# Optimization experiments

Measured on AMD Instinct MI355X. Metric: run time of the kernel, lower is better.

## Reference

```python
import jax, jax.numpy as jnp
import numpy as np

B, H, W, C, F = 32, 32, 32, 256, 64
K_NEIGH = 32  # L1 pixel-distance cutoff used for the static mask


def _distance_mask(h, w, k):
    # coords: [hw, 2] of (y, x); L1 pixel distances, normalized by max(h, w)
    ys, xs = jnp.meshgrid(jnp.arange(h), jnp.arange(w), indexing='ij')
    coords = jnp.stack([ys, xs], axis=-1).reshape(-1, 2).astype(jnp.float32)
    diff = jnp.abs(coords[:, None, :] - coords[None, :, :]).sum(-1)  # [hw, hw], == cdist p=1
    dist = diff / float(max(h, w))
    return jnp.where(diff <= k, dist, 0.0)


def setup_inputs() -> dict:
    key = jax.random.key(0)
    ks = jax.random.split(key, 7)
    return {
        'feature_map': jax.random.normal(ks[0], (B, H, W, C), dtype=jnp.float32),
        'emb_W': jax.random.normal(ks[1], (F, C), dtype=jnp.float32) * (1.0 / np.sqrt(C)),
        'emb_b': jax.random.normal(ks[2], (F,), dtype=jnp.float32) * 0.01,
        'attn_W': jax.random.normal(ks[3], (C, C), dtype=jnp.float32) * (1.0 / np.sqrt(C)),
        'attn_b': jax.random.normal(ks[4], (C,), dtype=jnp.float32) * 0.01,
        'thr_W': jax.random.normal(ks[5], (1, C), dtype=jnp.float32) * (1.0 / np.sqrt(C)),
        'thr_b': jax.random.normal(ks[6], (1,), dtype=jnp.float32) * 0.01,
        'layer': 0,
    }


def reference(feature_map, emb_W, emb_b, attn_W, attn_b, thr_W, thr_b, layer):
    b, h, w, c = feature_map.shape
    hw = h * w
    x = feature_map.reshape(b, hw, c)  # row-major (y, x) flatten, matches torch view

    # 1x1 conv -> per-pixel linear: instance embeddings [b, hw, F]
    emb = jnp.einsum('bnc,fc->bnf', x, emb_W) + emb_b

    # squared Euclidean pairwise distances (cdist p=2, then squared)
    sq = jnp.sum(emb * emb, axis=-1)  # [b, hw]
    d2 = jnp.maximum(sq[:, :, None] + sq[:, None, :]
                     - 2.0 * jnp.einsum('bnf,bmf->bnm', emb, emb), 0.0)

    mask = _distance_mask(h, w, K_NEIGH)  # [hw, hw] static buffer
    sim = jax.nn.softmax(jnp.exp(-d2) - (1.0 - mask), axis=-1)  # [b, hw, hw]

    # shortcut = attention_conv(feature_map): [b, hw, c]
    shortcut = jnp.einsum('bnc,dc->bnd', x, attn_W) + attn_b

    # per-pixel learned threshold: [b, hw]
    Tinst = (jnp.einsum('bnc,oc->bno', shortcut, thr_W) + thr_b)[..., 0]

    A = jax.nn.softmax(jnp.maximum(sim - Tinst[:, None, :], 0.0), axis=-1)

    # bmm: out[b, i, c] = sum_j shortcut[b, j, c] * A[b, i, j]
    attn_out = jnp.einsum('bjc,bij->bic', shortcut, A)

    res = (x + attn_out).reshape(b, h, w, c)
    return res
```

## Files before the change

kernel.cpp:

```cpp
#include <hip/hip_runtime.h>
#include <hip/hip_bf16.h>


typedef short bf16x8 __attribute__((ext_vector_type(8)));
typedef float f32x4 __attribute__((ext_vector_type(4)));

#define LOG2E 1.4426950408889634f

__device__ __forceinline__ unsigned short f2bf(float f) {
  unsigned u = __float_as_uint(f);
  u += 0x7fffu + ((u >> 16) & 1u);
  return (unsigned short)(u >> 16);
}
__device__ __forceinline__ float bf2f(unsigned short h) {
  return __uint_as_float(((unsigned)h) << 16);
}
__device__ __forceinline__ unsigned pack2(float a, float b) {
  return (unsigned)f2bf(a) | ((unsigned)f2bf(b) << 16);
}
__device__ __forceinline__ unsigned cvtpk(float lo, float hi) {
  unsigned r;
  asm("v_cvt_pk_bf16_f32 %0, %1, %2" : "=v"(r) : "v"(lo), "v"(hi));
  return r;
}
__device__ __forceinline__ float exp2x(float x) {
  float r;
  asm("v_exp_f32 %0, %1" : "=v"(r) : "v"(x));
  return r;
}
__device__ __forceinline__ f32x4 mfma16(bf16x8 a, bf16x8 b, f32x4 c) {
  return __builtin_amdgcn_mfma_f32_16x16x32_bf16(a, b, c, 0, 0, 0);
}
__device__ __forceinline__ int iabs(int v) { return v < 0 ? -v : v; }
__device__ __forceinline__ void load_lds16(const void* g, void* l) {
  __builtin_amdgcn_global_load_lds(
      (const __attribute__((address_space(1))) unsigned int*)g,
      (__attribute__((address_space(3))) unsigned int*)l, 16, 0, 0);
}

__global__ __launch_bounds__(256) void k_prep(const float* __restrict__ embW,
                                              const float* __restrict__ attnW,
                                              unsigned short* __restrict__ Wb) {
  const int i = (blockIdx.x * 256 + threadIdx.x) * 4;
  float4 v = (i < 16384) ? *(const float4*)(embW + i)
                         : *(const float4*)(attnW + (i - 16384));
  ushort4 p; p.x = f2bf(v.x); p.y = f2bf(v.y); p.z = f2bf(v.z); p.w = f2bf(v.w);
  *(ushort4*)(Wb + i) = p;
}

__global__ __launch_bounds__(256) void k_lin(const float* __restrict__ x,
                                             const unsigned short* __restrict__ Wb,
                                             const float* __restrict__ embB,
                                             const float* __restrict__ attnB,
                                             const float* __restrict__ thrW,
                                             const float* __restrict__ thrB,
                                             unsigned short* __restrict__ embb,
                                             float* __restrict__ sq2,
                                             unsigned short* __restrict__ scT,
                                             float* __restrict__ T2out) {
  __shared__ union {
    struct { unsigned short xs[64][40]; unsigned short ws[320][40]; } a;
    unsigned short St[256][72];
  } sm;
  const int t = threadIdx.x;
  const int Mbase = blockIdx.x * 64;
  const int lane = t & 63, wave = t >> 6;
  const int wm = wave >> 1, wn = wave & 1;
  const int l15 = lane & 15, quad = lane >> 4;

  f32x4 acc[2][10] = {};
  for (int k0 = 0; k0 < 256; k0 += 32) {
    {
      int row = t >> 2, c0 = (t & 3) * 8;
      const float* src = x + (size_t)(Mbase + row) * 256 + k0 + c0;
      float4 a = *(const float4*)src;
      float4 b = *(const float4*)(src + 4);
      uint4 p; p.x = pack2(a.x, a.y); p.y = pack2(a.z, a.w);
      p.z = pack2(b.x, b.y); p.w = pack2(b.z, b.w);
      *(uint4*)&sm.a.xs[row][c0] = p;
    }
    {
      const unsigned short* wsrc = Wb + (size_t)t * 256 + k0;
      for (int s = 0; s < 4; s++)
        *(uint4*)&sm.a.ws[t][s * 8] = *(const uint4*)(wsrc + s * 8);
      if (t < 64) {
        const unsigned short* wsrc2 = Wb + (size_t)(256 + t) * 256 + k0;
        for (int s = 0; s < 4; s++)
          *(uint4*)&sm.a.ws[256 + t][s * 8] = *(const uint4*)(wsrc2 + s * 8);
      }
    }
    __syncthreads();
    bf16x8 af[2];
    af[0] = *(const bf16x8*)&sm.a.xs[wm * 32 + l15][quad * 8];
    af[1] = *(const bf16x8*)&sm.a.xs[wm * 32 + 16 + l15][quad * 8];
    for (int nt = 0; nt < 10; nt++) {
      bf16x8 bfr = *(const bf16x8*)&sm.a.ws[wn * 160 + nt * 16 + l15][quad * 8];
      acc[0][nt] = mfma16(af[0], bfr, acc[0][nt]);
      acc[1][nt] = mfma16(af[1], bfr, acc[1][nt]);
    }
    __syncthreads();
  }

  if (wn == 0) {
    float sp[2][4] = {{0.f,0.f,0.f,0.f},{0.f,0.f,0.f,0.f}};
    for (int rt = 0; rt < 2; rt++)
      for (int nt = 0; nt < 4; nt++) {
        int n = nt * 16 + l15;
        float bias = embB[n];
        for (int r = 0; r < 4; r++) {
          float v = acc[rt][nt][r] + bias;
          unsigned short hb = f2bf(v);
          int row = wm * 32 + rt * 16 + quad * 4 + r;
          embb[(size_t)(Mbase + row) * 64 + n] = hb;
          float vf = bf2f(hb);
          sp[rt][r] += vf * vf;
        }
      }
    for (int m = 8; m >= 1; m >>= 1)
      for (int rt = 0; rt < 2; rt++)
        for (int r = 0; r < 4; r++)
          sp[rt][r] += __shfl_xor(sp[rt][r], m);
    if (l15 == 0)
      for (int rt = 0; rt < 2; rt++)
        for (int r = 0; r < 4; r++)
          sq2[Mbase + wm * 32 + rt * 16 + quad * 4 + r] = sp[rt][r] * LOG2E;
  }

  for (int rt = 0; rt < 2; rt++)
    for (int nt = 0; nt < 10; nt++) {
      int n = wn * 160 + nt * 16 + l15;
      if (n < 64) continue;
      int c = n - 64;
      float bias = attnB[c];
      for (int r = 0; r < 4; r++) {
        float v = acc[rt][nt][r] + bias;
        sm.St[c][wm * 32 + rt * 16 + quad * 4 + r] = f2bf(v);
      }
    }
  __syncthreads();

  const int b = Mbase >> 10, jbase = Mbase & 1023;
  {
    unsigned short* dst = scT + ((size_t)b * 256 + t) * 1024 + jbase;
    for (int s = 0; s < 8; s++)
      *(uint4*)(dst + s * 8) = *(const uint4*)&sm.St[t][s * 8];
  }
  {
    float tp = 0.f;
    int j = t >> 2, cs = (t & 3) * 64;
    for (int c = 0; c < 64; c++)
      tp += bf2f(sm.St[cs + c][j]) * thrW[cs + c];
    tp += __shfl_xor(tp, 1);
    tp += __shfl_xor(tp, 2);
    if ((t & 3) == 0) T2out[Mbase + j] = (tp + thrB[0]) * LOG2E;
  }
}

__global__ __launch_bounds__(512) void k_scores(const unsigned short* __restrict__ embb,
                                                const float* __restrict__ sq2,
                                                const float* __restrict__ T2,
                                                unsigned short* __restrict__ U,
                                                float* __restrict__ Z) {
  __shared__ unsigned short E_lds[16 * 1040];
  __shared__ float rbuf[16];
  __shared__ float lm2[64];
  const int t = threadIdx.x, lane = t & 63, wave = t >> 6;
  const int b = blockIdx.x >> 6, rb = (blockIdx.x & 63) * 16;
  const int l15 = lane & 15, quad = lane >> 4;
  const unsigned short* eb = embb + (size_t)b * 1024 * 64;
  const float* sq2b = sq2 + b * 1024;

  if (t < 16) rbuf[t] = 0.f;
  if (t < 64) {
    float m = (t <= 32) ? (float)t * (1.f / 32.f) : 0.f;
    lm2[t] = (m - 1.f) * LOG2E;
  }
  __syncthreads();

  const int i = rb + l15;
  bf16x8 if0 = *(const bf16x8*)(eb + (size_t)i * 64 + quad * 8);
  bf16x8 if1 = *(const bf16x8*)(eb + (size_t)i * 64 + 32 + quad * 8);
  const float nsq2i = -sq2b[i];
  const int yi = i >> 5, xi = i & 31;
  const int jq = wave * 128;
  float rp = 0.f;
  #pragma unroll
  for (int j0 = jq; j0 < jq + 128; j0 += 16) {
    const int jr = j0 + l15;
    bf16x8 jf0 = *(const bf16x8*)(eb + (size_t)jr * 64 + quad * 8);
    bf16x8 jf1 = *(const bf16x8*)(eb + (size_t)jr * 64 + 32 + quad * 8);
    f32x4 g = {0.f, 0.f, 0.f, 0.f};
    g = mfma16(jf0, if0, g);
    g = mfma16(jf1, if1, g);
    const int jg = j0 + quad * 4;
    const float4 s4 = *(const float4*)(sq2b + jg);
    const int dy = iabs(yi - (jg >> 5));
    const int dxa = xi - (jg & 31);
    float e0, e1, e2, e3;
    {
      float w2 = fminf(fmaf(2.f * LOG2E, g[0], nsq2i - s4.x), 0.f);
      e0 = exp2x(fmaf(exp2x(w2), LOG2E, lm2[dy + iabs(dxa)]));
      w2 = fminf(fmaf(2.f * LOG2E, g[1], nsq2i - s4.y), 0.f);
      e1 = exp2x(fmaf(exp2x(w2), LOG2E, lm2[dy + iabs(dxa - 1)]));
      w2 = fminf(fmaf(2.f * LOG2E, g[2], nsq2i - s4.z), 0.f);
      e2 = exp2x(fmaf(exp2x(w2), LOG2E, lm2[dy + iabs(dxa - 2)]));
      w2 = fminf(fmaf(2.f * LOG2E, g[3], nsq2i - s4.w), 0.f);
      e3 = exp2x(fmaf(exp2x(w2), LOG2E, lm2[dy + iabs(dxa - 3)]));
    }
    rp += (e0 + e1) + (e2 + e3);
    uint2 pk; pk.x = cvtpk(e0, e1); pk.y = cvtpk(e2, e3);
    *(uint2*)&E_lds[l15 * 1040 + jg] = pk;
  }
  rp += __shfl_xor(rp, 16);
  rp += __shfl_xor(rp, 32);
  __syncthreads();
  if (quad == 0) atomicAdd(&rbuf[l15], rp);
  __syncthreads();

  const int prow = t >> 5, seg = t & 31;
  const float invR2 = LOG2E / rbuf[prow];
  const float* T2b = T2 + b * 1024;
  unsigned short* ur = U + ((size_t)(b * 1024 + rb + prow)) * 1024;
  float z = 0.f;
  #pragma unroll
  for (int c = 0; c < 4; c++) {
    int j = c * 256 + seg * 8;
    union { bf16x8 v; unsigned short s[8]; } ev;
    ev.v = *(const bf16x8*)&E_lds[prow * 1040 + j];
    float4 t0 = *(const float4*)(T2b + j);
    float4 t1 = *(const float4*)(T2b + j + 4);
    float tf[8] = {t0.x, t0.y, t0.z, t0.w, t1.x, t1.y, t1.z, t1.w};
    uint4 uo;
    unsigned q[4];
    #pragma unroll
    for (int h = 0; h < 4; h++) {
      float u0 = exp2x(fmaxf(fmaf(bf2f(ev.s[2 * h]), invR2, -tf[2 * h]), 0.f));
      float u1 = exp2x(fmaxf(fmaf(bf2f(ev.s[2 * h + 1]), invR2, -tf[2 * h + 1]), 0.f));
      unsigned qq = cvtpk(u0, u1);
      q[h] = qq;
      z += __uint_as_float(qq << 16) + __uint_as_float(qq & 0xffff0000u);
    }
    uo.x = q[0]; uo.y = q[1]; uo.z = q[2]; uo.w = q[3];
    *(uint4*)(ur + j) = uo;
  }
  z += __shfl_xor(z, 1);
  z += __shfl_xor(z, 2);
  z += __shfl_xor(z, 4);
  z += __shfl_xor(z, 8);
  z += __shfl_xor(z, 16);
  if (seg == 0) Z[b * 1024 + rb + prow] = z;
}

__global__ __launch_bounds__(256) void k_out(const unsigned short* __restrict__ U,
                                             const float* __restrict__ Z,
                                             const unsigned short* __restrict__ scT,
                                             const float* __restrict__ x,
                                             float* __restrict__ out) {
  __shared__ unsigned short Ab[2][128 * 32];
  __shared__ unsigned short Bb[2][128 * 32];
  const int t = threadIdx.x, lane = t & 63, wave = t >> 6;
  const int wm = wave >> 1, wn = wave & 1;
  const int l15 = lane & 15, quad = lane >> 4;
  const int x8 = blockIdx.x & 7, s = blockIdx.x >> 3;
  const int b = x8 * 4 + (s >> 4), tile = s & 15;
  const int rb = (tile >> 1) * 128, cb = (tile & 1) * 128;

  const unsigned short* Ubase = U + (size_t)b * 1024 * 1024 + (size_t)rb * 1024;
  const unsigned short* Sbase = scT + (size_t)b * 256 * 1024 + (size_t)cb * 1024;

  const int c0 = wave * 64 + lane;
  const int c1 = c0 + 256;
  const int r0 = c0 >> 2, o0 = (c0 & 3) * 8;
  const int r1 = c1 >> 2, o1 = (c1 & 3) * 8;
  const unsigned short* ua0 = Ubase + (size_t)r0 * 1024 + o0;
  const unsigned short* ua1 = Ubase + (size_t)r1 * 1024 + o1;
  const unsigned short* sa0 = Sbase + (size_t)r0 * 1024 + o0;
  const unsigned short* sa1 = Sbase + (size_t)r1 * 1024 + o1;

#define STAGE(bufi, j0)                              \
  do {                                               \
    load_lds16(ua0 + (j0), &Ab[bufi][c0 * 8]);       \
    load_lds16(ua1 + (j0), &Ab[bufi][c1 * 8]);       \
    load_lds16(sa0 + (j0), &Bb[bufi][c0 * 8]);       \
    load_lds16(sa1 + (j0), &Bb[bufi][c1 * 8]);       \
  } while (0)

  f32x4 acc[4][4] = {};
  STAGE(0, 0);
  __syncthreads();
  int cur = 0;
  for (int it = 0; it < 32; ++it) {
    if (it < 31) STAGE(cur ^ 1, (it + 1) * 32);
    bf16x8 af[4], bfr[4];
    for (int i = 0; i < 4; i++)
      af[i] = *(const bf16x8*)&Ab[cur][(wm * 64 + i * 16 + l15) * 32 + quad * 8];
    for (int i = 0; i < 4; i++)
      bfr[i] = *(const bf16x8*)&Bb[cur][(wn * 64 + i * 16 + l15) * 32 + quad * 8];
    for (int i = 0; i < 4; i++)
      for (int j = 0; j < 4; j++)
        acc[i][j] = mfma16(af[i], bfr[j], acc[i][j]);
    if (it < 31) {
      __syncthreads();
      cur ^= 1;
    }
  }
#undef STAGE

  const int colb = cb + wn * 64;
  for (int i = 0; i < 4; i++) {
    int rowb = rb + wm * 64 + i * 16 + quad * 4;
    float iz[4];
    for (int r = 0; r < 4; r++) iz[r] = 1.f / Z[b * 1024 + rowb + r];
    for (int j = 0; j < 4; j++) {
      int c = colb + j * 16 + l15;
      for (int r = 0; r < 4; r++) {
        size_t idx = ((size_t)(b * 1024 + rowb + r)) * 256 + c;
        out[idx] = x[idx] + acc[i][j][r] * iz[r];
      }
    }
  }
}

extern "C" void kernel_launch(void* const* d_in, const int* in_sizes, int n_in,
                              void* d_out, int out_size, void* d_ws, size_t ws_size,
                              hipStream_t stream) {
  const float* x     = (const float*)d_in[0];
  const float* embW  = (const float*)d_in[1];
  const float* embB  = (const float*)d_in[2];
  const float* attnW = (const float*)d_in[3];
  const float* attnB = (const float*)d_in[4];
  const float* thrW  = (const float*)d_in[5];
  const float* thrB  = (const float*)d_in[6];
  float* out = (float*)d_out;

  char* ws = (char*)d_ws;
  unsigned short* embb = (unsigned short*)(ws);
  unsigned short* scT  = (unsigned short*)(ws + (4ull << 20));
  unsigned short* U    = (unsigned short*)(ws + (20ull << 20));
  unsigned short* Wb   = (unsigned short*)(ws + (36ull << 20));
  float* sq2 = (float*)(ws + (84ull << 20));
  float* T2  = (float*)(ws + (84ull << 20) + (128ull << 10));
  float* Z   = (float*)(ws + (84ull << 20) + (256ull << 10));

  k_prep<<<80, 256, 0, stream>>>(embW, attnW, Wb);
  k_lin<<<512, 256, 0, stream>>>(x, Wb, embB, attnB, thrW, thrB, embb, sq2, scT, T2);
  k_scores<<<2048, 512, 0, stream>>>(embb, sq2, T2, U, Z);
  k_out<<<512, 256, 0, stream>>>(U, Z, scT, x, out);
}
```

Before: 197.7 us.

## Fuse score recompute and second softmax into output GEMM, drop U matrix

Splits the score kernel into a row-sum-only pass (k_R) and fuses the exponent chain, threshold softmax numerator and row-sum Z into the final attention GEMM kernel. This avoids writing and re-reading the 64 MB bf16 U matrix in global memory, at the cost of recomputing the Gram MFMA and double exponentials a second time per tile. The mask lookup table is replaced by inline arithmetic, and the K tile is loaded with an XOR swizzle into LDS. The output kernel now handles all 256 columns per 64-row tile, with two barriers per iteration.

```diff
diff --git a/kernel.cpp b/kernel.cpp
--- a/kernel.cpp
+++ b/kernel.cpp
@@ -36,6 +36,14 @@
   __builtin_amdgcn_global_load_lds(
       (const __attribute__((address_space(1))) unsigned int*)g,
       (__attribute__((address_space(3))) unsigned int*)l, 16, 0, 0);
+}
+
+__device__ __forceinline__ float e_chain(float g, float nsq2i, float sq2j,
+                                         int diff) {
+  float w2 = fminf(fmaf(2.f * LOG2E, g, nsq2i - sq2j), 0.f);
+  float fd = (float)diff;
+  float fs = (diff <= 32) ? fd : 0.f;
+  return exp2x(fmaf(exp2x(w2), LOG2E, fmaf(fs, LOG2E / 32.f, -LOG2E)));
 }
 
 __global__ __launch_bounds__(256) void k_prep(const float* __restrict__ embW,
@@ -156,14 +164,10 @@
   }
 }
 
-__global__ __launch_bounds__(512) void k_scores(const unsigned short* __restrict__ embb,
-                                                const float* __restrict__ sq2,
-                                                const float* __restrict__ T2,
-                                                unsigned short* __restrict__ U,
-                                                float* __restrict__ Z) {
-  __shared__ unsigned short E_lds[16 * 1040];
+__global__ __launch_bounds__(512) void k_R(const unsigned short* __restrict__ embb,
+                                           const float* __restrict__ sq2,
+                                           float* __restrict__ R) {
   __shared__ float rbuf[16];
-  __shared__ float lm2[64];
   const int t = threadIdx.x, lane = t & 63, wave = t >> 6;
   const int b = blockIdx.x >> 6, rb = (blockIdx.x & 63) * 16;
   const int l15 = lane & 15, quad = lane >> 4;
@@ -171,10 +175,6 @@
   const float* sq2b = sq2 + b * 1024;
 
   if (t < 16) rbuf[t] = 0.f;
-  if (t < 64) {
-    float m = (t <= 32) ? (float)t * (1.f / 32.f) : 0.f;
-    lm2[t] = (m - 1.f) * LOG2E;
-  }
   __syncthreads();
 
   const int i = rb + l15;
@@ -184,7 +184,6 @@
   const int yi = i >> 5, xi = i & 31;
   const int jq = wave * 128;
   float rp = 0.f;
-  #pragma unroll
   for (int j0 = jq; j0 < jq + 128; j0 += 16) {
     const int jr = j0 + l15;
     bf16x8 jf0 = *(const bf16x8*)(eb + (size_t)jr * 64 + quad * 8);
@@ -196,126 +195,141 @@
     const float4 s4 = *(const float4*)(sq2b + jg);
     const int dy = iabs(yi - (jg >> 5));
     const int dxa = xi - (jg & 31);
-    float e0, e1, e2, e3;
-    {
-      float w2 = fminf(fmaf(2.f * LOG2E, g[0], nsq2i - s4.x), 0.f);
-      e0 = exp2x(fmaf(exp2x(w2), LOG2E, lm2[dy + iabs(dxa)]));
-      w2 = fminf(fmaf(2.f * LOG2E, g[1], nsq2i - s4.y), 0.f);
-      e1 = exp2x(fmaf(exp2x(w2), LOG2E, lm2[dy + iabs(dxa - 1)]));
-      w2 = fminf(fmaf(2.f * LOG2E, g[2], nsq2i - s4.z), 0.f);
-      e2 = exp2x(fmaf(exp2x(w2), LOG2E, lm2[dy + iabs(dxa - 2)]));
-      w2 = fminf(fmaf(2.f * LOG2E, g[3], nsq2i - s4.w), 0.f);
-      e3 = exp2x(fmaf(exp2x(w2), LOG2E, lm2[dy + iabs(dxa - 3)]));
-    }
+    float e0 = e_chain(g[0], nsq2i, s4.x, dy + iabs(dxa));
+    float e1 = e_chain(g[1], nsq2i, s4.y, dy + iabs(dxa - 1));
+    float e2 = e_chain(g[2], nsq2i, s4.z, dy + iabs(dxa - 2));
+    float e3 = e_chain(g[3], nsq2i, s4.w, dy + iabs(dxa - 3));
     rp += (e0 + e1) + (e2 + e3);
-    uint2 pk; pk.x = cvtpk(e0, e1); pk.y = cvtpk(e2, e3);
-    *(uint2*)&E_lds[l15 * 1040 + jg] = pk;
   }
   rp += __shfl_xor(rp, 16);
   rp += __shfl_xor(rp, 32);
-  __syncthreads();
   if (quad == 0) atomicAdd(&rbuf[l15], rp);
   __syncthreads();
-
-  const int prow = t >> 5, seg = t & 31;
-  const float invR2 = LOG2E / rbuf[prow];
+  if (t < 16) R[b * 1024 + rb + t] = rbuf[t];
+}
+
+__global__ __launch_bounds__(256) void k_out2(const unsigned short* __restrict__ embb,
+                                              const float* __restrict__ sq2,
+                                              const float* __restrict__ T2,
+                                              const float* __restrict__ Rv,
+                                              const unsigned short* __restrict__ scT,
+                                              const float* __restrict__ x,
+                                              float* __restrict__ out) {
+  __shared__ unsigned short Kb[2][32 * 64];
+  __shared__ unsigned short Sb[2][1024 * 8];
+  __shared__ unsigned short Pb[64 * 40];
+  __shared__ float zbuf[64];
+  const int t = threadIdx.x, lane = t & 63, w = t >> 6;
+  const int l15 = lane & 15, quad = lane >> 4;
+  const int b = blockIdx.x >> 4, rt = blockIdx.x & 15;
+  const unsigned short* eb = embb + (size_t)b * 1024 * 64;
+  const float* sq2b = sq2 + b * 1024;
   const float* T2b = T2 + b * 1024;
-  unsigned short* ur = U + ((size_t)(b * 1024 + rb + prow)) * 1024;
-  float z = 0.f;
+
+  const int qrow = w * 16 + l15;
+  const int gi = rt * 64 + qrow;
+  bf16x8 qf0 = *(const bf16x8*)(eb + (size_t)gi * 64 + quad * 8);
+  bf16x8 qf1 = *(const bf16x8*)(eb + (size_t)gi * 64 + 32 + quad * 8);
+  const float nsq2q = -sq2b[gi];
+  const float invR2 = LOG2E / Rv[b * 1024 + gi];
+  const int yi = gi >> 5, xi = gi & 31;
+
+  const int krow = t >> 3;
+  const int kchunk = (t & 7) ^ (krow & 7);
+  const unsigned short* srow = scT + ((size_t)b * 256 + t) * 1024;
+
+#define STAGE(bufi, j0s)                                                     \
+  do {                                                                       \
+    load_lds16(eb + (size_t)((j0s) + krow) * 64 + kchunk * 8,                \
+               &Kb[bufi][t * 8]);                                            \
+    load_lds16(srow + (j0s), &Sb[bufi][(0 * 256 + t) * 8]);                  \
+    load_lds16(srow + (j0s) + 8, &Sb[bufi][(1 * 256 + t) * 8]);              \
+    load_lds16(srow + (j0s) + 16, &Sb[bufi][(2 * 256 + t) * 8]);             \
+    load_lds16(srow + (j0s) + 24, &Sb[bufi][(3 * 256 + t) * 8]);             \
+  } while (0)
+
+  STAGE(0, 0);
+  __syncthreads();
+
+  f32x4 acc[4][4] = {};
+  float zloc = 0.f;
+  const int sw = l15 & 7;
+
+  for (int it = 0; it < 32; ++it) {
+    const int cur = it & 1;
+    const int j0 = it * 32;
+    if (it < 31) STAGE(cur ^ 1, j0 + 32);
+
+    bf16x8 kf00 = *(const bf16x8*)&Kb[cur][(l15) * 64 + ((0 * 4 + quad) ^ sw) * 8];
+    bf16x8 kf01 = *(const bf16x8*)&Kb[cur][(l15) * 64 + ((1 * 4 + quad) ^ sw) * 8];
+    bf16x8 kf10 = *(const bf16x8*)&Kb[cur][(16 + l15) * 64 + ((0 * 4 + quad) ^ sw) * 8];
+    bf16x8 kf11 = *(const bf16x8*)&Kb[cur][(16 + l15) * 64 + ((1 * 4 + quad) ^ sw) * 8];
+    f32x4 g0 = {0.f, 0.f, 0.f, 0.f}, g1 = {0.f, 0.f, 0.f, 0.f};
+    g0 = mfma16(kf00, qf0, g0);
+    g0 = mfma16(kf01, qf1, g0);
+    g1 = mfma16(kf10, qf0, g1);
+    g1 = mfma16(kf11, qf1, g1);
+
+    #pragma unroll
+    for (int jt = 0; jt < 2; ++jt) {
+      const f32x4 g = jt ? g1 : g0;
+      const int jg = j0 + jt * 16 + quad * 4;
+      const float4 s4 = *(const float4*)(sq2b + jg);
+      const float4 t4 = *(const float4*)(T2b + jg);
+      const int dy = iabs(yi - (jg >> 5));
+      const int dxa = xi - (jg & 31);
+      float e0 = e_chain(g[0], nsq2q, s4.x, dy + iabs(dxa));
+      float e1 = e_chain(g[1], nsq2q, s4.y, dy + iabs(dxa - 1));
+      float e2 = e_chain(g[2], nsq2q, s4.z, dy + iabs(dxa - 2));
+      float e3 = e_chain(g[3], nsq2q, s4.w, dy + iabs(dxa - 3));
+      float u0 = exp2x(fmaxf(fmaf(e0, invR2, -t4.x), 0.f));
+      float u1 = exp2x(fmaxf(fmaf(e1, invR2, -t4.y), 0.f));
+      float u2 = exp2x(fmaxf(fmaf(e2, invR2, -t4.z), 0.f));
+      float u3 = exp2x(fmaxf(fmaf(e3, invR2, -t4.w), 0.f));
+      unsigned pk0 = cvtpk(u0, u1);
+      unsigned pk1 = cvtpk(u2, u3);
+      zloc += __uint_as_float(pk0 << 16) + __uint_as_float(pk0 & 0xffff0000u);
+      zloc += __uint_as_float(pk1 << 16) + __uint_as_float(pk1 & 0xffff0000u);
+      uint2 pk; pk.x = pk0; pk.y = pk1;
+      *(uint2*)&Pb[qrow * 40 + jt * 16 + quad * 4] = pk;
+    }
+    __syncthreads();
+
+    bf16x8 af[4], bfv[4];
+    #pragma unroll
+    for (int i = 0; i < 4; i++)
+      af[i] = *(const bf16x8*)&Pb[(i * 16 + l15) * 40 + quad * 8];
+    #pragma unroll
+    for (int n = 0; n < 4; n++)
+      bfv[n] = *(const bf16x8*)&Sb[cur][(quad * 256 + w * 64 + n * 16 + l15) * 8];
+    #pragma unroll
+    for (int i = 0; i < 4; i++)
+      #pragma unroll
+      for (int n = 0; n < 4; n++)
+        acc[i][n] = mfma16(af[i], bfv[n], acc[i][n]);
+    __syncthreads();
+  }
+#undef STAGE
+
+  zloc += __shfl_xor(zloc, 16);
+  zloc += __shfl_xor(zloc, 32);
+  if (quad == 0) zbuf[qrow] = zloc;
+  __syncthreads();
+
   #pragma unroll
-  for (int c = 0; c < 4; c++) {
-    int j = c * 256 + seg * 8;
-    union { bf16x8 v; unsigned short s[8]; } ev;
-    ev.v = *(const bf16x8*)&E_lds[prow * 1040 + j];
-    float4 t0 = *(const float4*)(T2b + j);
-    float4 t1 = *(const float4*)(T2b + j + 4);
-    float tf[8] = {t0.x, t0.y, t0.z, t0.w, t1.x, t1.y, t1.z, t1.w};
-    uint4 uo;
-    unsigned q[4];
-    #pragma unroll
-    for (int h = 0; h < 4; h++) {
-      float u0 = exp2x(fmaxf(fmaf(bf2f(ev.s[2 * h]), invR2, -tf[2 * h]), 0.f));
-      float u1 = exp2x(fmaxf(fmaf(bf2f(ev.s[2 * h + 1]), invR2, -tf[2 * h + 1]), 0.f));
-      unsigned qq = cvtpk(u0, u1);
-      q[h] = qq;
-      z += __uint_as_float(qq << 16) + __uint_as_float(qq & 0xffff0000u);
-    }
-    uo.x = q[0]; uo.y = q[1]; uo.z = q[2]; uo.w = q[3];
-    *(uint4*)(ur + j) = uo;
-  }
-  z += __shfl_xor(z, 1);
-  z += __shfl_xor(z, 2);
-  z += __shfl_xor(z, 4);
-  z += __shfl_xor(z, 8);
-  z += __shfl_xor(z, 16);
-  if (seg == 0) Z[b * 1024 + rb + prow] = z;
-}
-
-__global__ __launch_bounds__(256) void k_out(const unsigned short* __restrict__ U,
-                                             const float* __restrict__ Z,
-                                             const unsigned short* __restrict__ scT,
-                                             const float* __restrict__ x,
-                                             float* __restrict__ out) {
-  __shared__ unsigned short Ab[2][128 * 32];
-  __shared__ unsigned short Bb[2][128 * 32];
-  const int t = threadIdx.x, lane = t & 63, wave = t >> 6;
-  const int wm = wave >> 1, wn = wave & 1;
-  const int l15 = lane & 15, quad = lane >> 4;
-  const int x8 = blockIdx.x & 7, s = blockIdx.x >> 3;
-  const int b = x8 * 4 + (s >> 4), tile = s & 15;
-  const int rb = (tile >> 1) * 128, cb = (tile & 1) * 128;
-
-  const unsigned short* Ubase = U + (size_t)b * 1024 * 1024 + (size_t)rb * 1024;
-  const unsigned short* Sbase = scT + (size_t)b * 256 * 1024 + (size_t)cb * 1024;
-
-  const int c0 = wave * 64 + lane;
-  const int c1 = c0 + 256;
-  const int r0 = c0 >> 2, o0 = (c0 & 3) * 8;
-  const int r1 = c1 >> 2, o1 = (c1 & 3) * 8;
-  const unsigned short* ua0 = Ubase + (size_t)r0 * 1024 + o0;
-  const unsigned short* ua1 = Ubase + (size_t)r1 * 1024 + o1;
-  const unsigned short* sa0 = Sbase + (size_t)r0 * 1024 + o0;
-  const unsigned short* sa1 = Sbase + (size_t)r1 * 1024 + o1;
-
-#define STAGE(bufi, j0)                              \
-  do {                                               \
-    load_lds16(ua0 + (j0), &Ab[bufi][c0 * 8]);       \
-    load_lds16(ua1 + (j0), &Ab[bufi][c1 * 8]);       \
-    load_lds16(sa0 + (j0), &Bb[bufi][c0 * 8]);       \
-    load_lds16(sa1 + (j0), &Bb[bufi][c1 * 8]);       \
-  } while (0)
-
-  f32x4 acc[4][4] = {};
-  STAGE(0, 0);
-  __syncthreads();
-  int cur = 0;
-  for (int it = 0; it < 32; ++it) {
-    if (it < 31) STAGE(cur ^ 1, (it + 1) * 32);
-    bf16x8 af[4], bfr[4];
-    for (int i = 0; i < 4; i++)
-      af[i] = *(const bf16x8*)&Ab[cur][(wm * 64 + i * 16 + l15) * 32 + quad * 8];
-    for (int i = 0; i < 4; i++)
-      bfr[i] = *(const bf16x8*)&Bb[cur][(wn * 64 + i * 16 + l15) * 32 + quad * 8];
-    for (int i = 0; i < 4; i++)
-      for (int j = 0; j < 4; j++)
-        acc[i][j] = mfma16(af[i], bfr[j], acc[i][j]);
-    if (it < 31) {
-      __syncthreads();
-      cur ^= 1;
-    }
-  }
-#undef STAGE
-
-  const int colb = cb + wn * 64;
   for (int i = 0; i < 4; i++) {
-    int rowb = rb + wm * 64 + i * 16 + quad * 4;
+    const int rowl = i * 16 + quad * 4;
     float iz[4];
-    for (int r = 0; r < 4; r++) iz[r] = 1.f / Z[b * 1024 + rowb + r];
-    for (int j = 0; j < 4; j++) {
-      int c = colb + j * 16 + l15;
+    #pragma unroll
+    for (int r = 0; r < 4; r++) iz[r] = 1.f / zbuf[rowl + r];
+    const int grow = b * 1024 + rt * 64 + rowl;
+    #pragma unroll
+    for (int n = 0; n < 4; n++) {
+      const int c = w * 64 + n * 16 + l15;
+      #pragma unroll
       for (int r = 0; r < 4; r++) {
-        size_t idx = ((size_t)(b * 1024 + rowb + r)) * 256 + c;
-        out[idx] = x[idx] + acc[i][j][r] * iz[r];
+        size_t idx = (size_t)(grow + r) * 256 + c;
+        out[idx] = x[idx] + acc[i][n][r] * iz[r];
       }
     }
   }
@@ -336,14 +350,13 @@
   char* ws = (char*)d_ws;
   unsigned short* embb = (unsigned short*)(ws);
   unsigned short* scT  = (unsigned short*)(ws + (4ull << 20));
-  unsigned short* U    = (unsigned short*)(ws + (20ull << 20));
-  unsigned short* Wb   = (unsigned short*)(ws + (36ull << 20));
+  unsigned short* Wb   = (unsigned short*)(ws + (20ull << 20));
   float* sq2 = (float*)(ws + (84ull << 20));
   float* T2  = (float*)(ws + (84ull << 20) + (128ull << 10));
-  float* Z   = (float*)(ws + (84ull << 20) + (256ull << 10));
+  float* Rv  = (float*)(ws + (84ull << 20) + (256ull << 10));
 
   k_prep<<<80, 256, 0, stream>>>(embW, attnW, Wb);
   k_lin<<<512, 256, 0, stream>>>(x, Wb, embB, attnB, thrW, thrB, embb, sq2, scT, T2);
-  k_scores<<<2048, 512, 0, stream>>>(embb, sq2, T2, U, Z);
-  k_out<<<512, 256, 0, stream>>>(U, Z, scT, x, out);
-}
+  k_R<<<2048, 512, 0, stream>>>(embb, sq2, Rv);
+  k_out2<<<512, 256, 0, stream>>>(embb, sq2, T2, Rv, scT, x, out);
+}
```

Measured after the change: 215.8 us. 9.1% more time.
